# Optimization experiments

Measured on AMD Instinct MI355X. Metric: run time of the kernel, lower is better.

## Reference

```python
import jax, jax.numpy as jnp
import numpy as np

EPS = 1e-05
# log-space init values matching the torch module (deterministic: use the means)
_S_MEANS = np.array([0.61803, 0.3904, 0.1174, 0.0606, 0.0308, 0.0155, 0.0078, 0.0039, 0.002, 0.0001], dtype=np.float32)


def setup_inputs() -> dict:
    key = jax.random.key(0)
    k1, k2 = jax.random.split(key)
    B, F, T = 16, 128, 2048
    x = jax.random.uniform(k1, (B, F, T), dtype=jnp.float32)  # nonneg spectrogram-like
    # perturb s means slightly like torch.normal(mean, 0.01*mean)
    noise = 1.0 + 0.01 * jax.random.normal(k2, (10,), dtype=jnp.float32)
    s_log = jnp.log(jnp.abs(jnp.asarray(_S_MEANS) * noise))
    alpha_log = jnp.full((F,), jnp.log(0.8), dtype=jnp.float32)
    delta_log = jnp.full((F,), jnp.log(10.0), dtype=jnp.float32)
    r_log = jnp.full((F,), jnp.log(0.25), dtype=jnp.float32)
    return {"x": x, "s_log": s_log, "alpha_log": alpha_log, "delta_log": delta_log, "r_log": r_log}


def _pcen(x, s_log, alpha_log, delta_log, r_log):
    # x: [B, F, T]
    s = jnp.exp(s_log)[:, None, None]        # [10,1,1]
    alpha = jnp.exp(alpha_log)[:, None]      # [F,1]
    delta = jnp.exp(delta_log)[:, None]      # [F,1]
    r = jnp.exp(r_log)[:, None]              # [F,1]

    x_t = jnp.moveaxis(x, -1, 0)             # [T, B, F]
    init = jnp.broadcast_to(x_t[0][None], (10,) + x_t[0].shape)  # [10,B,F]

    def step(carry, xt):
        carry = (1.0 - s) * carry + s * xt[None]  # [10,B,F]
        return carry, carry

    _, rest = jax.lax.scan(step, init, x_t[1:])
    smoother = jnp.concatenate([init[None], rest], axis=0)   # [T,10,B,F]
    smoother = jnp.moveaxis(smoother, 0, -1)                 # [10,B,F,T]

    log_eps = jnp.log(jnp.float32(EPS))
    smooth = jnp.exp(-alpha * (log_eps + jnp.log1p(smoother / EPS)))  # [10,B,F,T]
    pcen = (x[None] * smooth + delta) ** r - delta ** r              # [10,B,F,T]
    return jnp.transpose(pcen, (1, 0, 2, 3))                          # [B,10,F,T]


def reference(x, s_log, alpha_log, delta_log, r_log):
    return _pcen(x, s_log, alpha_log, delta_log, r_log)
```

## Files before the change

### kernel.cpp

```cpp
#include <hip/hip_runtime.h>

#define T_DIM 2048
#define F_DIM 128
#define B_DIM 16
#define NS 10
#define TPB 256
#define EPT 8

__device__ __forceinline__ float fast_exp2(float x) { return __builtin_amdgcn_exp2f(x); }
__device__ __forceinline__ float fast_log2(float x) { return __builtin_amdgcn_logf(x); }

__global__ __launch_bounds__(TPB) void pcen_kernel(
    const float* __restrict__ x,
    const float* __restrict__ s_log,
    const float* __restrict__ alpha_log,
    const float* __restrict__ delta_log,
    const float* __restrict__ r_log,
    float* __restrict__ out)
{
    const int bf   = blockIdx.x;
    const int b    = bf / F_DIM;
    const int f    = bf % F_DIM;
    const int tid  = threadIdx.x;
    const int lane = tid & 63;
    const int wave = tid >> 6;

    const float* xrow = x + (size_t)bf * T_DIM;

    float xv[EPT];
    {
        const float4* xr4 = (const float4*)(xrow + tid * EPT);
        float4 p0 = xr4[0];
        float4 p1 = xr4[1];
        xv[0] = p0.x; xv[1] = p0.y; xv[2] = p0.z; xv[3] = p0.w;
        xv[4] = p1.x; xv[5] = p1.y; xv[6] = p1.z; xv[7] = p1.w;
    }

    const float x0 = xrow[0];

    const float alpha   = expf(alpha_log[f]);
    const float delta   = expf(delta_log[f]);
    const float r       = expf(r_log[f]);
    const float delta_r = fast_exp2(r * fast_log2(delta));
    const float neg_alpha = -alpha;

    __shared__ float lds_m[4];
    __shared__ float lds_v[4];

    float* orow = out + (size_t)(b * NS) * (F_DIM * (size_t)T_DIM)
                      + (size_t)f * T_DIM + (size_t)tid * EPT;

    for (int si = 0; si < NS; ++si) {
        const float s = expf(s_log[si]);
        const float a = 1.0f - s;

        float c = 0.0f;
        #pragma unroll
        for (int i = 0; i < EPT; ++i) c = fmaf(a, c, s * xv[i]);
        const float a2 = a * a, a4 = a2 * a2, A8 = a4 * a4;

        float m = A8, v = c;
        #pragma unroll
        for (int d = 1; d < 64; d <<= 1) {
            float m_up = __shfl_up(m, d);
            float v_up = __shfl_up(v, d);
            if (lane >= d) { v = fmaf(m, v_up, v); m *= m_up; }
        }
        float m_e = __shfl_up(m, 1);
        float v_e = __shfl_up(v, 1);
        if (lane == 0) { m_e = 1.0f; v_e = 0.0f; }

        if (si) __syncthreads();
        if (lane == 63) { lds_m[wave] = m; lds_v[wave] = v; }
        __syncthreads();

        float cw = x0;
        for (int w = 0; w < wave; ++w) cw = fmaf(lds_m[w], cw, lds_v[w]);
        const float cin = fmaf(m_e, cw, v_e);

        float o[EPT];
        float cc = cin;
        #pragma unroll
        for (int i = 0; i < EPT; ++i) {
            cc = fmaf(a, cc, s * xv[i]);
            float smooth = fast_exp2(neg_alpha * fast_log2(cc + 1e-5f));
            float base   = fmaf(xv[i], smooth, delta);
            o[i] = fast_exp2(r * fast_log2(base)) - delta_r;
        }

        float4* ow = (float4*)(orow + (size_t)si * (F_DIM * T_DIM));
        ow[0] = make_float4(o[0], o[1], o[2], o[3]);
        ow[1] = make_float4(o[4], o[5], o[6], o[7]);
    }
}

extern "C" void kernel_launch(void* const* d_in, const int* in_sizes, int n_in,
                              void* d_out, int out_size, void* d_ws, size_t ws_size,
                              hipStream_t stream) {
    const float* x         = (const float*)d_in[0];
    const float* s_log     = (const float*)d_in[1];
    const float* alpha_log = (const float*)d_in[2];
    const float* delta_log = (const float*)d_in[3];
    const float* r_log     = (const float*)d_in[4];
    float* out = (float*)d_out;

    pcen_kernel<<<dim3(B_DIM * F_DIM), dim3(TPB), 0, stream>>>(
        x, s_log, alpha_log, delta_log, r_log, out);
}
```

Baseline: 184.3 us.

## Assign one wavefront per (row, smoothing coefficient) and scan tiles in-wave

Each wavefront now handles one (b,f) row for a single s value, replacing a block that looped over all ten s values with block-wide barriers. The row is split into 8 tiles of 256 elements, each scanned inside the wave with shuffle-based prefix sums that use precomputed powers of the decay. Tiles are then chained through a carried scalar. This removes the LDS and __syncthreads traffic and exposes ten times more independent work. The cost is that x is reloaded ten times, and each wave holds more registers for its 8 float4 tiles.

```diff
diff --git a/kernel.cpp b/kernel.cpp
--- a/kernel.cpp
+++ b/kernel.cpp
@@ -4,8 +4,8 @@
 #define F_DIM 128
 #define B_DIM 16
 #define NS 10
+#define NTILE 8
 #define TPB 256
-#define EPT 8
 
 __device__ __forceinline__ float fast_exp2(float x) { return __builtin_amdgcn_exp2f(x); }
 __device__ __forceinline__ float fast_log2(float x) { return __builtin_amdgcn_logf(x); }
@@ -18,79 +18,102 @@
     const float* __restrict__ r_log,
     float* __restrict__ out)
 {
-    const int bf   = blockIdx.x;
-    const int b    = bf / F_DIM;
-    const int f    = bf % F_DIM;
     const int tid  = threadIdx.x;
     const int lane = tid & 63;
-    const int wave = tid >> 6;
+    const int gw   = blockIdx.x * (TPB / 64) + (tid >> 6);
+    const int bf   = gw / NS;
+    const int si   = gw - bf * NS;
+    const int b    = bf >> 7;
+    const int f    = bf & (F_DIM - 1);
 
-    const float* xrow = x + (size_t)bf * T_DIM;
+    const float4* xrow = (const float4*)(x + (size_t)bf * T_DIM);
 
-    float xv[EPT];
+    float4 xv[NTILE];
+    #pragma unroll
+    for (int k = 0; k < NTILE; ++k) xv[k] = xrow[k * 64 + lane];
+
+    const float s  = expf(s_log[si]);
+    const float a  = 1.0f - s;
+    const float alpha = expf(alpha_log[f]);
+    const float delta = expf(delta_log[f]);
+    const float r     = expf(r_log[f]);
+    const float delta_r   = fast_exp2(r * fast_log2(delta));
+    const float neg_alpha = -alpha;
+
+    float pa[6];
     {
-        const float4* xr4 = (const float4*)(xrow + tid * EPT);
-        float4 p0 = xr4[0];
-        float4 p1 = xr4[1];
-        xv[0] = p0.x; xv[1] = p0.y; xv[2] = p0.z; xv[3] = p0.w;
-        xv[4] = p1.x; xv[5] = p1.y; xv[6] = p1.z; xv[7] = p1.w;
+        float a2 = a * a;
+        pa[0] = a2 * a2;
+        #pragma unroll
+        for (int bb = 1; bb < 6; ++bb) pa[bb] = pa[bb - 1] * pa[bb - 1];
+    }
+    const float a256 = pa[5] * pa[5];
+
+    float a4l = 1.0f;
+    #pragma unroll
+    for (int bb = 0; bb < 6; ++bb) a4l *= ((lane >> bb) & 1) ? pa[bb] : 1.0f;
+
+    float V[NTILE];
+    #pragma unroll
+    for (int k = 0; k < NTILE; ++k) {
+        float c = s * xv[k].x;
+        c = fmaf(a, c, s * xv[k].y);
+        c = fmaf(a, c, s * xv[k].z);
+        c = fmaf(a, c, s * xv[k].w);
+        V[k] = c;
     }
 
-    const float x0 = xrow[0];
+    #pragma unroll
+    for (int d = 1, bb = 0; d < 64; d <<= 1, ++bb) {
+        #pragma unroll
+        for (int k = 0; k < NTILE; ++k) {
+            float up = __shfl_up(V[k], d);
+            up = (lane >= d) ? up : 0.0f;
+            V[k] = fmaf(pa[bb], up, V[k]);
+        }
+    }
 
-    const float alpha   = expf(alpha_log[f]);
-    const float delta   = expf(delta_log[f]);
-    const float r       = expf(r_log[f]);
-    const float delta_r = fast_exp2(r * fast_log2(delta));
-    const float neg_alpha = -alpha;
+    float Ve[NTILE], Vl[NTILE];
+    #pragma unroll
+    for (int k = 0; k < NTILE; ++k) {
+        float e = __shfl_up(V[k], 1);
+        Ve[k] = (lane >= 1) ? e : 0.0f;
+        Vl[k] = __shfl(V[k], 63);
+    }
 
-    __shared__ float lds_m[4];
-    __shared__ float lds_v[4];
+    float tc = __shfl(xv[0].x, 0);
 
-    float* orow = out + (size_t)(b * NS) * (F_DIM * (size_t)T_DIM)
-                      + (size_t)f * T_DIM + (size_t)tid * EPT;
+    float* orow = out + (size_t)(((b * NS + si) * F_DIM) + f) * T_DIM;
 
-    for (int si = 0; si < NS; ++si) {
-        const float s = expf(s_log[si]);
-        const float a = 1.0f - s;
+    #pragma unroll
+    for (int k = 0; k < NTILE; ++k) {
+        float cc = fmaf(a4l, tc, Ve[k]);
+        const float4 xk = xv[k];
+        float4 o;
 
-        float c = 0.0f;
-        #pragma unroll
-        for (int i = 0; i < EPT; ++i) c = fmaf(a, c, s * xv[i]);
-        const float a2 = a * a, a4 = a2 * a2, A8 = a4 * a4;
+        cc = fmaf(a, cc, s * xk.x);
+        { float sm2 = fast_exp2(neg_alpha * fast_log2(cc + 1e-5f));
+          float base = fmaf(xk.x, sm2, delta);
+          o.x = fast_exp2(r * fast_log2(base)) - delta_r; }
 
-        float m = A8, v = c;
-        #pragma unroll
-        for (int d = 1; d < 64; d <<= 1) {
-            float m_up = __shfl_up(m, d);
-            float v_up = __shfl_up(v, d);
-            if (lane >= d) { v = fmaf(m, v_up, v); m *= m_up; }
-        }
-        float m_e = __shfl_up(m, 1);
-        float v_e = __shfl_up(v, 1);
-        if (lane == 0) { m_e = 1.0f; v_e = 0.0f; }
+        cc = fmaf(a, cc, s * xk.y);
+        { float sm2 = fast_exp2(neg_alpha * fast_log2(cc + 1e-5f));
+          float base = fmaf(xk.y, sm2, delta);
+          o.y = fast_exp2(r * fast_log2(base)) - delta_r; }
 
-        if (si) __syncthreads();
-        if (lane == 63) { lds_m[wave] = m; lds_v[wave] = v; }
-        __syncthreads();
+        cc = fmaf(a, cc, s * xk.z);
+        { float sm2 = fast_exp2(neg_alpha * fast_log2(cc + 1e-5f));
+          float base = fmaf(xk.z, sm2, delta);
+          o.z = fast_exp2(r * fast_log2(base)) - delta_r; }
 
-        float cw = x0;
-        for (int w = 0; w < wave; ++w) cw = fmaf(lds_m[w], cw, lds_v[w]);
-        const float cin = fmaf(m_e, cw, v_e);
+        cc = fmaf(a, cc, s * xk.w);
+        { float sm2 = fast_exp2(neg_alpha * fast_log2(cc + 1e-5f));
+          float base = fmaf(xk.w, sm2, delta);
+          o.w = fast_exp2(r * fast_log2(base)) - delta_r; }
 
-        float o[EPT];
-        float cc = cin;
-        #pragma unroll
-        for (int i = 0; i < EPT; ++i) {
-            cc = fmaf(a, cc, s * xv[i]);
-            float smooth = fast_exp2(neg_alpha * fast_log2(cc + 1e-5f));
-            float base   = fmaf(xv[i], smooth, delta);
-            o[i] = fast_exp2(r * fast_log2(base)) - delta_r;
-        }
+        tc = fmaf(a256, tc, Vl[k]);
 
-        float4* ow = (float4*)(orow + (size_t)si * (F_DIM * T_DIM));
-        ow[0] = make_float4(o[0], o[1], o[2], o[3]);
-        ow[1] = make_float4(o[4], o[5], o[6], o[7]);
+        ((float4*)orow)[k * 64 + lane] = o;
     }
 }
 
@@ -104,6 +127,9 @@
     const float* r_log     = (const float*)d_in[4];
     float* out = (float*)d_out;
 
-    pcen_kernel<<<dim3(B_DIM * F_DIM), dim3(TPB), 0, stream>>>(
+    const int total_waves = B_DIM * F_DIM * NS;
+    const int blocks = total_waves / (TPB / 64);
+
+    pcen_kernel<<<dim3(blocks), dim3(TPB), 0, stream>>>(
         x, s_log, alpha_log, delta_log, r_log, out);
 }
```

Result: slower. 188.8 us (+2.5%).
